# Optimization experiments

Hardware: AMD Instinct MI355X
Metric: run time of the kernel (lower is better)

The kernel has to match this reference:

```python
import jax, jax.numpy as jnp
import numpy as np

N_NODES = 100000
N_EDGES = 600000
D_IN = 128
D_OUT = 128
N_REL = 16
N_BASES = 8


def setup_inputs() -> dict:
    key = jax.random.key(0)
    ks = jax.random.split(key, 6)
    x = jax.random.normal(ks[0], (N_NODES, D_IN), dtype=jnp.float32)
    edge_index = jax.random.randint(ks[1], (2, N_EDGES), 0, N_NODES, dtype=jnp.int64)
    edge_type = jax.random.randint(ks[2], (N_EDGES,), 0, N_REL, dtype=jnp.int64)
    # xavier-uniform-ish init scales
    b_lim = float(np.sqrt(6.0 / (D_IN + D_OUT)))
    c_lim = float(np.sqrt(6.0 / (N_REL + N_BASES)))
    w_lim = float(np.sqrt(6.0 / (D_IN + D_OUT)))
    bases = jax.random.uniform(ks[3], (N_BASES, D_IN, D_OUT), jnp.float32, -b_lim, b_lim)
    coefficients = jax.random.uniform(ks[4], (N_REL, N_BASES), jnp.float32, -c_lim, c_lim)
    w_self = jax.random.uniform(ks[5], (D_OUT, D_IN), jnp.float32, -w_lim, w_lim)
    return {"x": x, "edge_index": edge_index, "edge_type": edge_type,
            "bases": bases, "coefficients": coefficients, "w_self": w_self}


def reference(x, edge_index, edge_type, bases, coefficients, w_self):
    # self loop: Linear(in, out, bias=False) -> x @ W^T
    out = x @ w_self.T  # [N, D_OUT]
    # relation weights from basis decomposition
    weights = jnp.einsum('rb,bio->rio', coefficients, bases)  # [R, D_IN, D_OUT]
    row, col = edge_index[0], edge_index[1]
    xc = x[col]  # [E, D_IN] gather of source features
    n_rel = weights.shape[0]
    msg = jnp.zeros((xc.shape[0], w_self.shape[0]), dtype=x.dtype)
    # fixed small loop over relations; masked accumulate matches per-relation grouped GEMM
    for r in range(n_rel):
        sel = (edge_type == r)[:, None]
        msg = msg + jnp.where(sel, xc @ weights[r], jnp.zeros((), x.dtype))
    # scatter-add messages to destination rows
    out = out.at[row].add(msg)
    return out
```

## Files before the change

kernel.cpp:

```cpp
#include <hip/hip_runtime.h>

#define NN 100000
#define NE 600000
#define ET (NE + NN)
#define D 128
#define NREL 16
#define NSLICE 8
#define SLICE_N 12500
#define BPS 17
#define NBIN (NSLICE * BPS)
#define SCANB 391
#define TPB 4
#define MAXSLICET (NE / 64 + 16 + SLICE_N / 64 + 1)
#define GEMMG (NSLICE * ((MAXSLICET + TPB - 1) / TPB))
#define WGRID 1088

typedef short short8 __attribute__((ext_vector_type(8)));
typedef float f32x4 __attribute__((ext_vector_type(4)));
typedef unsigned int u32x4 __attribute__((ext_vector_type(4)));

#define C0 0
#define O0 136
#define CU0 273
#define T0 409

#define WT_OFF   0
#define META_OFF 557056
#define DH_OFF   559616
#define DO_OFF   959616
#define DC_OFF   1359624
#define BS_OFF   1759624
#define SCP_OFF  1761632
#define SR_OFF   7362144
#define XB_OFF   10162144
#define MSGB_OFF 35762144
#define MSGA_OFF 10162144
#define NEED_B   (MSGB_OFF + (size_t)ET * 128 * 2)
#define NEED_A   (MSGA_OFF + (size_t)ET * 128 * 2)

__device__ __forceinline__ unsigned short f2bf(float f) {
  unsigned u = __builtin_bit_cast(unsigned, f);
  u += 0x7fffu + ((u >> 16) & 1u);
  return (unsigned short)(u >> 16);
}

__device__ __forceinline__ void lds_barrier() {
  asm volatile("s_waitcnt lgkmcnt(0)" ::: "memory");
  __builtin_amdgcn_s_barrier();
}

__global__ __launch_bounds__(256) void k_prep(const float* __restrict__ bases,
    const float* __restrict__ coef, const float* __restrict__ w_self,
    unsigned short* __restrict__ wT, const float* __restrict__ x,
    unsigned short* __restrict__ xb)
{
  if (blockIdx.x < WGRID) {
    int idx = blockIdx.x * 256 + threadIdx.x;
    int r = idx >> 14;
    int t = idx & 16383;
    float v;
    if (r < 16) {
      int o = t >> 7, i = t & 127;
      float acc = 0.f;
      #pragma unroll
      for (int b = 0; b < 8; ++b)
        acc += coef[r * 8 + b] * bases[b * 16384 + i * 128 + o];
      v = acc;
    } else {
      v = w_self[t];
    }
    wT[idx] = f2bf(v);
  } else {
    int i = (blockIdx.x - WGRID) * 256 + threadIdx.x;
    if (i >= NN * D / 4) return;
    f32x4 f = __builtin_nontemporal_load((const f32x4*)(x + (size_t)i * 4));
    unsigned short s0 = f2bf(f[0]), s1 = f2bf(f[1]), s2 = f2bf(f[2]), s3 = f2bf(f[3]);
    unsigned long long pk = (unsigned long long)s0 | ((unsigned long long)s1 << 16)
                          | ((unsigned long long)s2 << 32) | ((unsigned long long)s3 << 48);
    *(unsigned long long*)(xb + (size_t)i * 4) = pk;
  }
}

__global__ __launch_bounds__(256) void k_hist(const int* __restrict__ ei,
    const int* __restrict__ et, int* __restrict__ meta, int* __restrict__ dstHist)
{
  __shared__ int h[NBIN];
  int tid = threadIdx.x;
  if (tid < NBIN) h[tid] = 0;
  __syncthreads();
  for (int e = blockIdx.x * 256 + tid; e < NE; e += gridDim.x * 256) {
    int src = ei[NE + e];
    atomicAdd(&h[(src / SLICE_N) * BPS + et[e]], 1);
    atomicAdd(&dstHist[ei[e]], 1);
  }
  __syncthreads();
  if (tid < NBIN) atomicAdd(&meta[C0 + tid], h[tid]);
}

__global__ __launch_bounds__(256) void k_scan1(const int* __restrict__ dstHist,
    int* __restrict__ dstOff, int* __restrict__ blockSums)
{
  __shared__ int sh[256];
  int tid = threadIdx.x;
  int d = blockIdx.x * 256 + tid;
  int v = (d < NN) ? (dstHist[d] + 1) : 0;
  sh[tid] = v;
  __syncthreads();
  #pragma unroll
  for (int ofs = 1; ofs < 256; ofs <<= 1) {
    int t = (tid >= ofs) ? sh[tid - ofs] : 0;
    __syncthreads();
    sh[tid] += t;
    __syncthreads();
  }
  if (d < NN) dstOff[d] = sh[tid] - v;
  if (tid == 255) blockSums[blockIdx.x] = sh[tid];
}

__global__ __launch_bounds__(512) void k_scan2(int* __restrict__ blockSums, int* __restrict__ meta)
{
  __shared__ int sh[SCANB];
  int tid = threadIdx.x;
  if (tid < SCANB) sh[tid] = blockSums[tid];
  __syncthreads();
  if (tid == 0) {
    int run = 0;
    for (int i = 0; i < SCANB; ++i) { int c = sh[i]; sh[i] = run; run += c; }
    #pragma unroll
    for (int s = 0; s < NSLICE; ++s) meta[C0 + s * BPS + 16] = SLICE_N;
    int off = 0, toff = 0;
    for (int bn = 0; bn < NBIN; ++bn) {
      meta[O0 + bn] = off;
      meta[CU0 + bn] = off;
      meta[T0 + bn] = toff;
      int c = meta[C0 + bn];
      off += c;
      toff += (c + 63) >> 6;
    }
    meta[O0 + NBIN] = off;
    meta[T0 + NBIN] = toff;
  }
  __syncthreads();
  if (tid < SCANB) blockSums[tid] = sh[tid];
}

__global__ __launch_bounds__(256) void k_scan3(int* __restrict__ dstOff,
    const int* __restrict__ blockSums, int* __restrict__ dstCursor,
    int2* __restrict__ sCP, const int* __restrict__ meta)
{
  int tid = threadIdx.x;
  int d = blockIdx.x * 256 + tid;
  int base = blockSums[blockIdx.x];
  if (d < NN) {
    int o = dstOff[d] + base;
    dstOff[d] = o;
    dstCursor[d] = o + 1;
    int s = d / SLICE_N;
    int pos = meta[O0 + s * BPS + 16] + (d - s * SLICE_N);
    sCP[pos] = make_int2(d, o);
  }
  if (d == NN) dstOff[NN] = ET;
}

__global__ __launch_bounds__(256) void k_self0(int2* __restrict__ sCP, int* __restrict__ sRow,
    const int* __restrict__ meta)
{
  int n = blockIdx.x * 256 + threadIdx.x;
  if (n < NN) {
    int s = n / SLICE_N;
    int pos = meta[O0 + s * BPS + 16] + (n - s * SLICE_N);
    sCP[pos] = make_int2(n, 0);
    sRow[pos] = n;
  }
}

__global__ __launch_bounds__(256) void k_scatter(const int* __restrict__ ei, const int* __restrict__ et,
    int* __restrict__ meta, int2* __restrict__ sCP, int* __restrict__ sRow,
    int* __restrict__ dstCursor, int doMsg)
{
  __shared__ int h[NBIN], base[NBIN], lh[NBIN];
  int tid = threadIdx.x;
  int start = blockIdx.x * 4096;
  int end = min(NE, start + 4096);
  if (tid < NBIN) { h[tid] = 0; lh[tid] = 0; }
  __syncthreads();
  for (int e = start + tid; e < end; e += 256) {
    int src = ei[NE + e];
    atomicAdd(&h[(src / SLICE_N) * BPS + et[e]], 1);
  }
  __syncthreads();
  if (tid < NBIN) base[tid] = atomicAdd(&meta[CU0 + tid], h[tid]);
  __syncthreads();
  for (int e = start + tid; e < end; e += 256) {
    int src = ei[NE + e];
    int bin = (src / SLICE_N) * BPS + et[e];
    int row = ei[e];
    int pos = base[bin] + atomicAdd(&lh[bin], 1);
    int slot = doMsg ? atomicAdd(&dstCursor[row], 1) : 0;
    sCP[pos] = make_int2(src, slot);
    if (!doMsg) sRow[pos] = row;
  }
}

__global__ __launch_bounds__(256) void k_gemm(const float* __restrict__ xf,
    const unsigned short* __restrict__ xb,
    const unsigned short* __restrict__ wT, const int* __restrict__ meta,
    const int2* __restrict__ sCP, const int* __restrict__ sRow,
    unsigned short* __restrict__ msg, float* __restrict__ out,
    int xbf, int msgmode)
{
  __shared__ short As[64 * 17 * 8];
  __shared__ short Es[64 * 136];
  __shared__ int Pos2[2][64];
  __shared__ int Rows[64];
  __shared__ int Cw[BPS], Ow[BPS], Tw[BPS + 1];

  int tid = threadIdx.x;
  int sl = blockIdx.x & 7;
  int chunk = blockIdx.x >> 3;
  if (tid < BPS) Cw[tid] = meta[C0 + sl * BPS + tid];
  if (tid >= 32 && tid < 32 + BPS) Ow[tid - 32] = meta[O0 + sl * BPS + (tid - 32)];
  if (tid >= 64 && tid < 64 + BPS + 1) Tw[tid - 64] = meta[T0 + sl * BPS + (tid - 64)];
  __syncthreads();
  int tile0 = Tw[0];
  int sliceNT = Tw[BPS] - tile0;
  int lt0 = chunk * TPB;
  if (lt0 >= sliceNT) return;

  int lane = tid & 63, wave = tid >> 6;
  int q = lane >> 4, l15 = lane & 15;
  int m = tid >> 2, ug = tid & 3;

  if (xbf && msgmode) {
    int j = 0;
    short8 pfS[4]; int cyS; bool vS; int rS, nrS;
    int2 cpG; bool vG; int rG, nrG;
    int2 cpP; bool vP; int rP, nrP;

    {
      int b = tile0 + lt0;
      while (j < 16 && Tw[j + 1] <= b) ++j;
      int e0 = Ow[j] + (b - Tw[j]) * 64;
      nrS = min(64, Ow[j] + Cw[j] - e0);
      rS = j;
      vS = m < nrS;
      int2 cp = sCP[vS ? (e0 + m) : e0];
      cyS = cp.y;
      const unsigned short* xr = xb + (size_t)cp.x * 128;
      #pragma unroll
      for (int s = 0; s < 4; ++s) {
        short8 v = (short8)(short)0;
        if (vS) v = *(const short8*)(xr + (ug * 4 + s) * 8);
        pfS[s] = v;
      }
    }
    if (TPB > 1 && lt0 + 1 < sliceNT) {
      int b = tile0 + lt0 + 1;
      while (j < 16 && Tw[j + 1] <= b) ++j;
      int e0 = Ow[j] + (b - Tw[j]) * 64;
      nrG = min(64, Ow[j] + Cw[j] - e0);
      rG = j;
      vG = m < nrG;
      cpG = sCP[vG ? (e0 + m) : e0];
    } else { vG = false; nrG = 0; rG = rS; cpG = make_int2(0, 0); }

    int rprev = -1;
    short8 bfr[2][4];
    for (int ti = 0; ti < TPB; ++ti) {
      int lt = lt0 + ti;
      if (lt >= sliceNT) break;
      int curR = rS, curNr = nrS;

      #pragma unroll
      for (int s = 0; s < 4; ++s)
        *(short8*)&As[(m * 17 + ug * 4 + s) * 8] = pfS[s];
      if (ug == 0) Pos2[ti & 1][m] = vS ? cyS : 0;

      if (ti + 2 < TPB && lt + 2 < sliceNT) {
        int bp = tile0 + lt + 2;
        while (j < 16 && Tw[j + 1] <= bp) ++j;
        int e0 = Ow[j] + (bp - Tw[j]) * 64;
        nrP = min(64, Ow[j] + Cw[j] - e0);
        rP = j;
        vP = m < nrP;
        cpP = sCP[vP ? (e0 + m) : e0];
      } else { vP = false; nrP = 0; rP = rG; cpP = make_int2(0, 0); }

      short8 pfN[4];
      {
        const unsigned short* xr = xb + (size_t)cpG.x * 128;
        #pragma unroll
        for (int s = 0; s < 4; ++s) {
          short8 v = (short8)(short)0;
          if (vG) v = *(const short8*)(xr + (ug * 4 + s) * 8);
          pfN[s] = v;
        }
      }

      if (curR != rprev) {
        const unsigned short* wr = wT + curR * 16384;
        #pragma unroll
        for (int ns = 0; ns < 2; ++ns)
          #pragma unroll
          for (int kk = 0; kk < 4; ++kk)
            bfr[ns][kk] = *(const short8*)(wr + (wave * 32 + ns * 16 + l15) * 128 + kk * 32 + q * 8);
        rprev = curR;
      }

      lds_barrier();

      f32x4 acc[4][2];
      #pragma unroll
      for (int ms = 0; ms < 4; ++ms)
        #pragma unroll
        for (int ns = 0; ns < 2; ++ns)
          acc[ms][ns] = (f32x4){0.f, 0.f, 0.f, 0.f};
      #pragma unroll
      for (int kk = 0; kk < 4; ++kk) {
        short8 af[4];
        #pragma unroll
        for (int ms = 0; ms < 4; ++ms)
          af[ms] = *(const short8*)&As[((ms * 16 + l15) * 17 + kk * 4 + q) * 8];
        #pragma unroll
        for (int ms = 0; ms < 4; ++ms)
          #pragma unroll
          for (int ns = 0; ns < 2; ++ns)
            acc[ms][ns] = __builtin_amdgcn_mfma_f32_16x16x32_bf16(af[ms], bfr[ns][kk], acc[ms][ns], 0, 0, 0);
      }

      #pragma unroll
      for (int ms = 0; ms < 4; ++ms)
        #pragma unroll
        for (int ns = 0; ns < 2; ++ns)
          #pragma unroll
          for (int reg = 0; reg < 4; ++reg)
            Es[(ms * 16 + q * 4 + reg) * 136 + wave * 32 + ns * 16 + l15] =
                (short)f2bf(acc[ms][ns][reg]);

      lds_barrier();

      #pragma unroll
      for (int i = 0; i < 4; ++i) {
        int row = wave * 16 + i * 4 + q;
        short8 v = *(const short8*)&Es[row * 136 + l15 * 8];
        if (row < curNr)
          __builtin_nontemporal_store(v,
              (short8*)(msg + (size_t)Pos2[ti & 1][row] * 128 + l15 * 8));
      }

      #pragma unroll
      for (int s = 0; s < 4; ++s) pfS[s] = pfN[s];
      cyS = cpG.y; vS = vG; rS = rG; nrS = nrG;
      cpG = cpP;   vG = vP; rG = rP; nrG = nrP;
    }
    return;
  }

  int rprev = -1;
  short8 bfr[2][4];
  for (int ti = 0; ti < TPB; ++ti) {
    int lt = lt0 + ti;
    if (lt >= sliceNT) break;
    int b = tile0 + lt;
    int j = 0;
    while (j < 16 && Tw[j + 1] <= b) ++j;
    int e0 = Ow[j] + (b - Tw[j]) * 64;
    int nrows = min(64, Ow[j] + Cw[j] - e0);

    bool valid = m < nrows;
    int e = valid ? (e0 + m) : e0;
    int2 cp = sCP[e];
    if (ug == 0) {
      Pos2[0][m] = valid ? cp.y : 0;
      if (!msgmode) Rows[m] = valid ? sRow[e] : 0;
    }
    int c = cp.x;
    if (xbf) {
      const unsigned short* xr = xb + (size_t)c * 128;
      #pragma unroll
      for (int s = 0; s < 4; ++s) {
        int u = ug * 4 + s;
        short8 pk = (short8)(short)0;
        if (valid) pk = *(const short8*)(xr + u * 8);
        *(short8*)&As[(m * 17 + u) * 8] = pk;
      }
    } else {
      const float* xr = xf + (size_t)c * 128;
      #pragma unroll
      for (int s = 0; s < 4; ++s) {
        int u = ug * 4 + s;
        float4 f0 = make_float4(0.f, 0.f, 0.f, 0.f), f1 = f0;
        if (valid) {
          f0 = *(const float4*)(xr + u * 8);
          f1 = *(const float4*)(xr + u * 8 + 4);
        }
        short8 pk;
        pk[0] = (short)f2bf(f0.x); pk[1] = (short)f2bf(f0.y);
        pk[2] = (short)f2bf(f0.z); pk[3] = (short)f2bf(f0.w);
        pk[4] = (short)f2bf(f1.x); pk[5] = (short)f2bf(f1.y);
        pk[6] = (short)f2bf(f1.z); pk[7] = (short)f2bf(f1.w);
        *(short8*)&As[(m * 17 + u) * 8] = pk;
      }
    }
    __syncthreads();

    if (j != rprev) {
      const unsigned short* wr = wT + j * 16384;
      #pragma unroll
      for (int ns = 0; ns < 2; ++ns)
        #pragma unroll
        for (int kk = 0; kk < 4; ++kk)
          bfr[ns][kk] = *(const short8*)(wr + (wave * 32 + ns * 16 + l15) * 128 + kk * 32 + q * 8);
      rprev = j;
    }

    f32x4 acc[4][2];
    #pragma unroll
    for (int ms = 0; ms < 4; ++ms)
      #pragma unroll
      for (int ns = 0; ns < 2; ++ns)
        acc[ms][ns] = (f32x4){0.f, 0.f, 0.f, 0.f};
    #pragma unroll
    for (int kk = 0; kk < 4; ++kk) {
      short8 af[4];
      #pragma unroll
      for (int ms = 0; ms < 4; ++ms)
        af[ms] = *(const short8*)&As[((ms * 16 + l15) * 17 + kk * 4 + q) * 8];
      #pragma unroll
      for (int ms = 0; ms < 4; ++ms)
        #pragma unroll
        for (int ns = 0; ns < 2; ++ns)
          acc[ms][ns] = __builtin_amdgcn_mfma_f32_16x16x32_bf16(af[ms], bfr[ns][kk], acc[ms][ns], 0, 0, 0);
    }

    if (msgmode) {
      __syncthreads();
      #pragma unroll
      for (int ms = 0; ms < 4; ++ms)
        #pragma unroll
        for (int ns = 0; ns < 2; ++ns)
          #pragma unroll
          for (int reg = 0; reg < 4; ++reg)
            Es[(ms * 16 + q * 4 + reg) * 136 + wave * 32 + ns * 16 + l15] =
                (short)f2bf(acc[ms][ns][reg]);
      __syncthreads();
      #pragma unroll
      for (int i = 0; i < 4; ++i) {
        int row = wave * 16 + i * 4 + q;
        short8 v = *(const short8*)&Es[row * 136 + l15 * 8];
        if (row < nrows)
          __builtin_nontemporal_store(v,
              (short8*)(msg + (size_t)Pos2[0][row] * 128 + l15 * 8));
      }
      __syncthreads();
    } else {
      #pragma unroll
      for (int ms = 0; ms < 4; ++ms)
        #pragma unroll
        for (int reg = 0; reg < 4; ++reg) {
          int mrow = ms * 16 + q * 4 + reg;
          if (mrow < nrows) {
            float* op = out + (size_t)Rows[mrow] * 128 + wave * 32 + l15;
            unsafeAtomicAdd(op, acc[ms][0][reg]);
            unsafeAtomicAdd(op + 16, acc[ms][1][reg]);
          }
        }
      __syncthreads();
    }
  }
}

__global__ __launch_bounds__(256) void k_reduce(const unsigned short* __restrict__ msg,
    const int* __restrict__ dstOff, float* __restrict__ out)
{
  int d = blockIdx.x * 16 + (threadIdx.x >> 4);
  if (d >= NN) return;
  int sl = threadIdx.x & 15;
  int s = dstOff[d], e = dstOff[d + 1];
  const unsigned short* base = msg + (size_t)sl * 8;
  float a[8], bacc[8];
  #pragma unroll
  for (int i = 0; i < 8; ++i) { a[i] = 0.f; bacc[i] = 0.f; }
  int j = s;
  for (; j + 1 < e; j += 2) {
    u32x4 v0 = __builtin_nontemporal_load((const u32x4*)(base + (size_t)j * 128));
    u32x4 v1 = __builtin_nontemporal_load((const u32x4*)(base + (size_t)(j + 1) * 128));
    #pragma unroll
    for (int c = 0; c < 4; ++c) {
      a[2 * c]     += __builtin_bit_cast(float, v0[c] << 16);
      a[2 * c + 1] += __builtin_bit_cast(float, v0[c] & 0xffff0000u);
      bacc[2 * c]     += __builtin_bit_cast(float, v1[c] << 16);
      bacc[2 * c + 1] += __builtin_bit_cast(float, v1[c] & 0xffff0000u);
    }
  }
  if (j < e) {
    u32x4 v0 = __builtin_nontemporal_load((const u32x4*)(base + (size_t)j * 128));
    #pragma unroll
    for (int c = 0; c < 4; ++c) {
      a[2 * c]     += __builtin_bit_cast(float, v0[c] << 16);
      a[2 * c + 1] += __builtin_bit_cast(float, v0[c] & 0xffff0000u);
    }
  }
  f32x4 w0, w1;
  w0[0] = a[0] + bacc[0]; w0[1] = a[1] + bacc[1]; w0[2] = a[2] + bacc[2]; w0[3] = a[3] + bacc[3];
  w1[0] = a[4] + bacc[4]; w1[1] = a[5] + bacc[5]; w1[2] = a[6] + bacc[6]; w1[3] = a[7] + bacc[7];
  float* op = out + (size_t)d * 128 + sl * 8;
  __builtin_nontemporal_store(w0, (f32x4*)op);
  __builtin_nontemporal_store(w1, (f32x4*)(op + 4));
}

extern "C" void kernel_launch(void* const* d_in, const int* in_sizes, int n_in,
                              void* d_out, int out_size, void* d_ws, size_t ws_size,
                              hipStream_t stream)
{
  const float* x      = (const float*)d_in[0];
  const int*   ei     = (const int*)d_in[1];
  const int*   et     = (const int*)d_in[2];
  const float* bases  = (const float*)d_in[3];
  const float* coef   = (const float*)d_in[4];
  const float* w_self = (const float*)d_in[5];
  float* out = (float*)d_out;
  char* ws = (char*)d_ws;
  unsigned short* wT = (unsigned short*)(ws + WT_OFF);
  int* meta      = (int*)(ws + META_OFF);
  int* dstHist   = (int*)(ws + DH_OFF);
  int* dstOff    = (int*)(ws + DO_OFF);
  int* dstCursor = (int*)(ws + DC_OFF);
  int* blockSums = (int*)(ws + BS_OFF);
  int2* sCP      = (int2*)(ws + SCP_OFF);
  int* sRow      = (int*)(ws + SR_OFF);
  unsigned short* xb = (unsigned short*)(ws + XB_OFF);

  const int modeB = (ws_size >= NEED_B) ? 1 : 0;
  const int modeA = (modeB || ws_size >= NEED_A) ? 1 : 0;
  unsigned short* msg = (unsigned short*)(ws + (modeB ? MSGB_OFF : MSGA_OFF));

  hipMemsetAsync(ws + META_OFF, 0, 2560 + 400000, stream);
  k_prep<<<modeB ? (WGRID + 12500) : WGRID, 256, 0, stream>>>(bases, coef, w_self, wT, x, xb);
  k_hist<<<256, 256, 0, stream>>>(ei, et, meta, dstHist);
  if (modeA) {
    k_scan1<<<SCANB, 256, 0, stream>>>(dstHist, dstOff, blockSums);
    k_scan2<<<1, 512, 0, stream>>>(blockSums, meta);
    k_scan3<<<SCANB, 256, 0, stream>>>(dstOff, blockSums, dstCursor, sCP, meta);
  } else {
    k_scan2<<<1, 512, 0, stream>>>(blockSums, meta);
    k_self0<<<SCANB, 256, 0, stream>>>(sCP, sRow, meta);
    hipMemsetAsync(d_out, 0, (size_t)NN * D * 4, stream);
  }
  k_scatter<<<(NE + 4095) / 4096, 256, 0, stream>>>(ei, et, meta, sCP, sRow, dstCursor, modeA);
  k_gemm<<<GEMMG, 256, 0, stream>>>(x, xb, wT, meta, sCP, sRow, msg, out, modeB, modeA);
  if (modeA)
    k_reduce<<<(NN + 15) / 16, 256, 0, stream>>>(msg, dstOff, out);
}
```

Measured before the change: 332.6 us.

## Bin edges by relation and destination slice, precompute GEMM tile table

Edges are now binned relation-major with 64 destination slices, where before they were grouped by 8 source slices. Message writes into the destination-ordered buffer become more local, and each relation's weights are reloaded far less often. A new k_tinfo kernel binary-searches the tile prefix once per tile and stores (start, rows, relation), so the GEMM uses a flat grid instead of per-slice chunks and a linear bin search. The cost is many more bins (1088), which means more partially filled 64-row tiles, one extra small launch, and weaker locality on the source-feature gather.

Result: slower. 367.3 us (+10.5%).

```diff
diff --git a/kernel.cpp b/kernel.cpp
--- a/kernel.cpp
+++ b/kernel.cpp
@@ -5,14 +5,15 @@
 #define ET (NE + NN)
 #define D 128
 #define NREL 16
-#define NSLICE 8
-#define SLICE_N 12500
-#define BPS 17
-#define NBIN (NSLICE * BPS)
+#define NDS 64
+#define DSL 1563
+#define NBIN (NREL * NDS + NDS)
+#define SELF0 (NREL * NDS)
 #define SCANB 391
 #define TPB 4
-#define MAXSLICET (NE / 64 + 16 + SLICE_N / 64 + 1)
-#define GEMMG (NSLICE * ((MAXSLICET + TPB - 1) / TPB))
+#define MAXTILES 12544
+#define GEMMG ((MAXTILES + TPB - 1) / TPB)
+#define TINFOG ((MAXTILES + 255) / 256)
 #define WGRID 1088
 
 typedef short short8 __attribute__((ext_vector_type(8)));
@@ -20,21 +21,22 @@
 typedef unsigned int u32x4 __attribute__((ext_vector_type(4)));
 
 #define C0 0
-#define O0 136
-#define CU0 273
-#define T0 409
+#define O0 1088
+#define CU0 2177
+#define T0 3265
 
 #define WT_OFF   0
 #define META_OFF 557056
-#define DH_OFF   559616
-#define DO_OFF   959616
-#define DC_OFF   1359624
-#define BS_OFF   1759624
-#define SCP_OFF  1761632
-#define SR_OFF   7362144
-#define XB_OFF   10162144
-#define MSGB_OFF 35762144
-#define MSGA_OFF 10162144
+#define DH_OFF   574592
+#define TI_OFF   574592
+#define DO_OFF   974592
+#define DC_OFF   1374600
+#define BS_OFF   1774600
+#define SCP_OFF  1776176
+#define XB_OFF   7376688
+#define SR_OFF   7376688
+#define MSGA_OFF 7376688
+#define MSGB_OFF 32976688
 #define NEED_B   (MSGB_OFF + (size_t)ET * 128 * 2)
 #define NEED_A   (MSGA_OFF + (size_t)ET * 128 * 2)
 
@@ -86,15 +88,16 @@
 {
   __shared__ int h[NBIN];
   int tid = threadIdx.x;
-  if (tid < NBIN) h[tid] = 0;
+  for (int i = tid; i < NBIN; i += 256) h[i] = 0;
   __syncthreads();
   for (int e = blockIdx.x * 256 + tid; e < NE; e += gridDim.x * 256) {
-    int src = ei[NE + e];
-    atomicAdd(&h[(src / SLICE_N) * BPS + et[e]], 1);
-    atomicAdd(&dstHist[ei[e]], 1);
-  }
-  __syncthreads();
-  if (tid < NBIN) atomicAdd(&meta[C0 + tid], h[tid]);
+    int dst = ei[e];
+    atomicAdd(&h[et[e] * NDS + dst / DSL], 1);
+    atomicAdd(&dstHist[dst], 1);
+  }
+  __syncthreads();
+  for (int i = tid; i < NBIN; i += 256)
+    if (h[i]) atomicAdd(&meta[C0 + i], h[i]);
 }
 
 __global__ __launch_bounds__(256) void k_scan1(const int* __restrict__ dstHist,
@@ -126,8 +129,8 @@
   if (tid == 0) {
     int run = 0;
     for (int i = 0; i < SCANB; ++i) { int c = sh[i]; sh[i] = run; run += c; }
-    #pragma unroll
-    for (int s = 0; s < NSLICE; ++s) meta[C0 + s * BPS + 16] = SLICE_N;
+    for (int s = 0; s < NDS; ++s)
+      meta[C0 + SELF0 + s] = min(DSL, NN - s * DSL);
     int off = 0, toff = 0;
     for (int bn = 0; bn < NBIN; ++bn) {
       meta[O0 + bn] = off;
@@ -155,8 +158,8 @@
     int o = dstOff[d] + base;
     dstOff[d] = o;
     dstCursor[d] = o + 1;
-    int s = d / SLICE_N;
-    int pos = meta[O0 + s * BPS + 16] + (d - s * SLICE_N);
+    int s = d / DSL;
+    int pos = meta[O0 + SELF0 + s] + (d - s * DSL);
     sCP[pos] = make_int2(d, o);
   }
   if (d == NN) dstOff[NN] = ET;
@@ -167,8 +170,8 @@
 {
   int n = blockIdx.x * 256 + threadIdx.x;
   if (n < NN) {
-    int s = n / SLICE_N;
-    int pos = meta[O0 + s * BPS + 16] + (n - s * SLICE_N);
+    int s = n / DSL;
+    int pos = meta[O0 + SELF0 + s] + (n - s * DSL);
     sCP[pos] = make_int2(n, 0);
     sRow[pos] = n;
   }
@@ -182,30 +185,48 @@
   int tid = threadIdx.x;
   int start = blockIdx.x * 4096;
   int end = min(NE, start + 4096);
-  if (tid < NBIN) { h[tid] = 0; lh[tid] = 0; }
+  for (int i = tid; i < NBIN; i += 256) { h[i] = 0; lh[i] = 0; }
   __syncthreads();
   for (int e = start + tid; e < end; e += 256) {
-    int src = ei[NE + e];
-    atomicAdd(&h[(src / SLICE_N) * BPS + et[e]], 1);
-  }
-  __syncthreads();
-  if (tid < NBIN) base[tid] = atomicAdd(&meta[CU0 + tid], h[tid]);
+    atomicAdd(&h[et[e] * NDS + ei[e] / DSL], 1);
+  }
+  __syncthreads();
+  for (int i = tid; i < NBIN; i += 256)
+    if (h[i]) base[i] = atomicAdd(&meta[CU0 + i], h[i]);
   __syncthreads();
   for (int e = start + tid; e < end; e += 256) {
-    int src = ei[NE + e];
-    int bin = (src / SLICE_N) * BPS + et[e];
     int row = ei[e];
+    int bin = et[e] * NDS + row / DSL;
     int pos = base[bin] + atomicAdd(&lh[bin], 1);
     int slot = doMsg ? atomicAdd(&dstCursor[row], 1) : 0;
-    sCP[pos] = make_int2(src, slot);
+    sCP[pos] = make_int2(ei[NE + e], slot);
     if (!doMsg) sRow[pos] = row;
   }
+}
+
+__global__ __launch_bounds__(256) void k_tinfo(const int* __restrict__ meta,
+    int4* __restrict__ tinfo)
+{
+  int t = blockIdx.x * 256 + threadIdx.x;
+  if (t >= MAXTILES) return;
+  int ntiles = meta[T0 + NBIN];
+  if (t >= ntiles) { tinfo[t] = make_int4(0, 0, 0, 0); return; }
+  int lo = 0, hi = NBIN;
+  while (lo < hi) {
+    int mid = (lo + hi + 1) >> 1;
+    if (meta[T0 + mid] <= t) lo = mid; else hi = mid - 1;
+  }
+  int bin = lo;
+  int e0 = meta[O0 + bin] + (t - meta[T0 + bin]) * 64;
+  int nr = min(64, meta[O0 + bin] + meta[C0 + bin] - e0);
+  tinfo[t] = make_int4(e0, nr, bin >> 6, 0);
 }
 
 __global__ __launch_bounds__(256) void k_gemm(const float* __restrict__ xf,
     const unsigned short* __restrict__ xb,
     const unsigned short* __restrict__ wT, const int* __restrict__ meta,
     const int2* __restrict__ sCP, const int* __restrict__ sRow,
+    const int4* __restrict__ tinfo,
     unsigned short* __restrict__ msg, float* __restrict__ out,
     int xbf, int msgmode)
 {
@@ -213,38 +234,26 @@
   __shared__ short Es[64 * 136];
   __shared__ int Pos2[2][64];
   __shared__ int Rows[64];
-  __shared__ int Cw[BPS], Ow[BPS], Tw[BPS + 1];
 
   int tid = threadIdx.x;
-  int sl = blockIdx.x & 7;
-  int chunk = blockIdx.x >> 3;
-  if (tid < BPS) Cw[tid] = meta[C0 + sl * BPS + tid];
-  if (tid >= 32 && tid < 32 + BPS) Ow[tid - 32] = meta[O0 + sl * BPS + (tid - 32)];
-  if (tid >= 64 && tid < 64 + BPS + 1) Tw[tid - 64] = meta[T0 + sl * BPS + (tid - 64)];
-  __syncthreads();
-  int tile0 = Tw[0];
-  int sliceNT = Tw[BPS] - tile0;
-  int lt0 = chunk * TPB;
-  if (lt0 >= sliceNT) return;
+  int ntiles = meta[T0 + NBIN];
+  int b0 = blockIdx.x * TPB;
+  if (b0 >= ntiles) return;
 
   int lane = tid & 63, wave = tid >> 6;
   int q = lane >> 4, l15 = lane & 15;
   int m = tid >> 2, ug = tid & 3;
 
   if (xbf && msgmode) {
-    int j = 0;
-    short8 pfS[4]; int cyS; bool vS; int rS, nrS;
-    int2 cpG; bool vG; int rG, nrG;
-    int2 cpP; bool vP; int rP, nrP;
+    short8 pfS[4]; int cyS; bool vS; int relS, nrS;
+    int2 cpG; bool vG; int relG, nrG;
+    int2 cpP; bool vP; int relP, nrP;
 
     {
-      int b = tile0 + lt0;
-      while (j < 16 && Tw[j + 1] <= b) ++j;
-      int e0 = Ow[j] + (b - Tw[j]) * 64;
-      nrS = min(64, Ow[j] + Cw[j] - e0);
-      rS = j;
+      int4 ifo = tinfo[b0];
+      nrS = ifo.y; relS = ifo.z;
       vS = m < nrS;
-      int2 cp = sCP[vS ? (e0 + m) : e0];
+      int2 cp = sCP[vS ? (ifo.x + m) : ifo.x];
       cyS = cp.y;
       const unsigned short* xr = xb + (size_t)cp.x * 128;
       #pragma unroll
@@ -254,37 +263,31 @@
         pfS[s] = v;
       }
     }
-    if (TPB > 1 && lt0 + 1 < sliceNT) {
-      int b = tile0 + lt0 + 1;
-      while (j < 16 && Tw[j + 1] <= b) ++j;
-      int e0 = Ow[j] + (b - Tw[j]) * 64;
-      nrG = min(64, Ow[j] + Cw[j] - e0);
-      rG = j;
+    if (TPB > 1 && b0 + 1 < ntiles) {
+      int4 ifo = tinfo[b0 + 1];
+      nrG = ifo.y; relG = ifo.z;
       vG = m < nrG;
-      cpG = sCP[vG ? (e0 + m) : e0];
-    } else { vG = false; nrG = 0; rG = rS; cpG = make_int2(0, 0); }
+      cpG = sCP[vG ? (ifo.x + m) : ifo.x];
+    } else { vG = false; nrG = 0; relG = relS; cpG = make_int2(0, 0); }
 
     int rprev = -1;
     short8 bfr[2][4];
     for (int ti = 0; ti < TPB; ++ti) {
-      int lt = lt0 + ti;
-      if (lt >= sliceNT) break;
-      int curR = rS, curNr = nrS;
+      int lt = b0 + ti;
+      if (lt >= ntiles) break;
+      int curR = relS, curNr = nrS;
 
       #pragma unroll
       for (int s = 0; s < 4; ++s)
         *(short8*)&As[(m * 17 + ug * 4 + s) * 8] = pfS[s];
       if (ug == 0) Pos2[ti & 1][m] = vS ? cyS : 0;
 
-      if (ti + 2 < TPB && lt + 2 < sliceNT) {
-        int bp = tile0 + lt + 2;
-        while (j < 16 && Tw[j + 1] <= bp) ++j;
-        int e0 = Ow[j] + (bp - Tw[j]) * 64;
-        nrP = min(64, Ow[j] + Cw[j] - e0);
-        rP = j;
+      if (ti + 2 < TPB && lt + 2 < ntiles) {
+        int4 ifo = tinfo[lt + 2];
+        nrP = ifo.y; relP = ifo.z;
         vP = m < nrP;
-        cpP = sCP[vP ? (e0 + m) : e0];
-      } else { vP = false; nrP = 0; rP = rG; cpP = make_int2(0, 0); }
+        cpP = sCP[vP ? (ifo.x + m) : ifo.x];
+      } else { vP = false; nrP = 0; relP = relG; cpP = make_int2(0, 0); }
 
       short8 pfN[4];
       {
@@ -350,8 +353,8 @@
 
       #pragma unroll
       for (int s = 0; s < 4; ++s) pfS[s] = pfN[s];
-      cyS = cpG.y; vS = vG; rS = rG; nrS = nrG;
-      cpG = cpP;   vG = vP; rG = rP; nrG = nrP;
+      cyS = cpG.y; vS = vG; relS = relG; nrS = nrG;
+      cpG = cpP;   vG = vP; relG = relP; nrG = nrP;
     }
     return;
   }
@@ -359,13 +362,10 @@
   int rprev = -1;
   short8 bfr[2][4];
   for (int ti = 0; ti < TPB; ++ti) {
-    int lt = lt0 + ti;
-    if (lt >= sliceNT) break;
-    int b = tile0 + lt;
-    int j = 0;
-    while (j < 16 && Tw[j + 1] <= b) ++j;
-    int e0 = Ow[j] + (b - Tw[j]) * 64;
-    int nrows = min(64, Ow[j] + Cw[j] - e0);
+    int lt = b0 + ti;
+    if (lt >= ntiles) break;
+    int4 ifo = tinfo[lt];
+    int e0 = ifo.x, nrows = ifo.y, rel = ifo.z;
 
     bool valid = m < nrows;
     int e = valid ? (e0 + m) : e0;
@@ -404,14 +404,14 @@
     }
     __syncthreads();
 
-    if (j != rprev) {
-      const unsigned short* wr = wT + j * 16384;
+    if (rel != rprev) {
+      const unsigned short* wr = wT + rel * 16384;
       #pragma unroll
       for (int ns = 0; ns < 2; ++ns)
         #pragma unroll
         for (int kk = 0; kk < 4; ++kk)
           bfr[ns][kk] = *(const short8*)(wr + (wave * 32 + ns * 16 + l15) * 128 + kk * 32 + q * 8);
-      rprev = j;
+      rprev = rel;
     }
 
     f32x4 acc[4][2];
@@ -524,6 +524,7 @@
   unsigned short* wT = (unsigned short*)(ws + WT_OFF);
   int* meta      = (int*)(ws + META_OFF);
   int* dstHist   = (int*)(ws + DH_OFF);
+  int4* tinfo    = (int4*)(ws + TI_OFF);
   int* dstOff    = (int*)(ws + DO_OFF);
   int* dstCursor = (int*)(ws + DC_OFF);
   int* blockSums = (int*)(ws + BS_OFF);
@@ -535,7 +536,7 @@
   const int modeA = (modeB || ws_size >= NEED_A) ? 1 : 0;
   unsigned short* msg = (unsigned short*)(ws + (modeB ? MSGB_OFF : MSGA_OFF));
 
-  hipMemsetAsync(ws + META_OFF, 0, 2560 + 400000, stream);
+  hipMemsetAsync(ws + META_OFF, 0, 17536 + 400000, stream);
   k_prep<<<modeB ? (WGRID + 12500) : WGRID, 256, 0, stream>>>(bases, coef, w_self, wT, x, xb);
   k_hist<<<256, 256, 0, stream>>>(ei, et, meta, dstHist);
   if (modeA) {
@@ -548,7 +549,8 @@
     hipMemsetAsync(d_out, 0, (size_t)NN * D * 4, stream);
   }
   k_scatter<<<(NE + 4095) / 4096, 256, 0, stream>>>(ei, et, meta, sCP, sRow, dstCursor, modeA);
-  k_gemm<<<GEMMG, 256, 0, stream>>>(x, xb, wT, meta, sCP, sRow, msg, out, modeB, modeA);
+  k_tinfo<<<TINFOG, 256, 0, stream>>>(meta, tinfo);
+  k_gemm<<<GEMMG, 256, 0, stream>>>(x, xb, wT, meta, sCP, sRow, tinfo, msg, out, modeB, modeA);
   if (modeA)
     k_reduce<<<(NN + 15) / 16, 256, 0, stream>>>(msg, dstOff, out);
 }
```
